# Optimization experiments

Measured on AMD Instinct MI355X. Metric: run time of the kernel, lower is better.

Reference implementation:

```python
import jax, jax.numpy as jnp
import numpy as np

N_NODES, N_EDGES = 50000, 800000
IN_DIM, OUT_DIM, EDGE_DIM = 128, 128, 32
NUM_HEADS = 8
HEAD_DIM = OUT_DIM // NUM_HEADS
SCALE = HEAD_DIM ** -0.5


def setup_inputs() -> dict:
    key = jax.random.key(0)
    ks = jax.random.split(key, 8)
    def lin_w(k, fan_in, fan_out):
        # kaiming-uniform-ish init like nn.Linear
        bound = 1.0 / np.sqrt(fan_in)
        return jax.random.uniform(k, (fan_in, fan_out), jnp.float32, -bound, bound)
    return {
        "node_features": jax.random.normal(ks[0], (N_NODES, IN_DIM), jnp.float32),
        "edge_features": jax.random.normal(ks[1], (N_EDGES, EDGE_DIM), jnp.float32),
        "Wq": lin_w(ks[2], IN_DIM, OUT_DIM), "bq": jnp.zeros((OUT_DIM,), jnp.float32),
        "Wk": lin_w(ks[3], IN_DIM, OUT_DIM), "bk": jnp.zeros((OUT_DIM,), jnp.float32),
        "Wv": lin_w(ks[4], IN_DIM, OUT_DIM), "bv": jnp.zeros((OUT_DIM,), jnp.float32),
        "We": lin_w(ks[5], EDGE_DIM, OUT_DIM), "be": jnp.zeros((OUT_DIM,), jnp.float32),
        "edge_list": jax.random.randint(ks[6], (N_EDGES, 2), 0, N_NODES, jnp.int32),
        "num_nodes": N_NODES,
    }


def reference(node_features, edge_features, Wq, bq, Wk, bk, Wv, bv, We, be, edge_list, num_nodes):
    # node projections -> [N, H, D]
    Q = (node_features @ Wq + bq).reshape(-1, NUM_HEADS, HEAD_DIM)
    K = (node_features @ Wk + bk).reshape(-1, NUM_HEADS, HEAD_DIM)
    V = (node_features @ Wv + bv).reshape(-1, NUM_HEADS, HEAD_DIM)
    edge_bias = (edge_features @ We + be).reshape(-1, NUM_HEADS, HEAD_DIM)

    src = edge_list[:, 0]  # node_in
    dst = edge_list[:, 1]  # node_out

    # per-edge per-head scores: [E, H]
    scores = jnp.einsum("ehd,ehd->eh", Q[src], K[dst]) * SCALE + edge_bias.sum(-1)
    # NOTE: softmax over the HEADS axis (dim=1), exactly as in the source
    weights = jax.nn.softmax(scores, axis=1)

    # weighted messages gathered from src, scattered to dst: [E, H, D] -> [N, H, D]
    msg = V[src] * weights[..., None]
    node_updates = jax.ops.segment_sum(msg, dst, num_segments=num_nodes)
    return node_updates.reshape(num_nodes, OUT_DIM)
```

## Files before the change

### kernel.cpp

```cpp
#include <hip/hip_runtime.h>
#include <math.h>

#define IN_DIM   128
#define OUT_DIM  128
#define EDGE_DIM 32
#define NUM_HEADS 8
#define HEAD_DIM 16
#define SCALE 0.25f
#define CSTRIDE 16
#define MAXDEG 48

typedef __attribute__((ext_vector_type(8))) short bf16x8;
typedef __attribute__((ext_vector_type(4))) float f32x4;
typedef __attribute__((ext_vector_type(2))) float f32x2;
typedef __attribute__((ext_vector_type(4))) unsigned int u32x4;

__device__ inline unsigned short f2bf(float x) {
    unsigned int u = __float_as_uint(x);
    unsigned int r = u + 0x7fff + ((u >> 16) & 1);
    return (unsigned short)(r >> 16);
}
__device__ inline float bflo(unsigned int u) { return __uint_as_float(u << 16); }
__device__ inline float bfhi(unsigned int u) { return __uint_as_float(u & 0xffff0000u); }
__device__ inline f32x2 up2(unsigned int u) {
    f32x2 r; r[0] = bflo(u); r[1] = bfhi(u); return r;
}

__global__ __launch_bounds__(256) void setup_kernel(
    int* __restrict__ counts, int n_nodes, int nbz,
    const float* __restrict__ Wq, const float* __restrict__ Wk,
    const float* __restrict__ Wv, unsigned short* __restrict__ WtB, int nbw,
    const float* __restrict__ We, const float* __restrict__ be,
    float* __restrict__ WeR, float* __restrict__ beR)
{
    const int bx = blockIdx.x;
    const int t  = threadIdx.x;
    if (bx < nbz) {
        const int i = bx * 256 + t;
        if (i < n_nodes) counts[i << 4] = 0;
    } else if (bx < nbz + nbw) {
        const int idx = (bx - nbz) * 256 + t;
        const int mat = idx >> 14;
        const int rem = idx & 16383;
        const int n = rem >> 7, k = rem & 127;
        const float* W = (mat == 0) ? Wq : (mat == 1) ? Wk : Wv;
        WtB[mat * 16384 + n * 128 + k] = f2bf(W[k * 128 + n]);
    } else {
        const int k = t >> 3, h = t & 7;
        float s = 0.f;
#pragma unroll
        for (int d = 0; d < HEAD_DIM; ++d) s += We[k * OUT_DIM + h * HEAD_DIM + d];
        WeR[k * NUM_HEADS + h] = s;
        if (t < NUM_HEADS) {
            float sb = 0.f;
#pragma unroll
            for (int d = 0; d < HEAD_DIM; ++d) sb += be[t * HEAD_DIM + d];
            beR[t] = sb;
        }
    }
}

__global__ __launch_bounds__(256) void mega_kernel(
    const float* __restrict__ X, const unsigned short* __restrict__ WtB,
    const float* __restrict__ bq, const float* __restrict__ bk,
    const float* __restrict__ bv,
    unsigned short* __restrict__ QVb, unsigned short* __restrict__ Kb,
    int n_nodes, int nbm,
    const int* __restrict__ el, int* __restrict__ counts,
    const float* __restrict__ ef, const float* __restrict__ WeR,
    const float* __restrict__ beR, unsigned int* __restrict__ recs,
    int n_edges)
{
    __shared__ unsigned short shW[16384];
    const int bx = blockIdx.x;
    const int t  = threadIdx.x;
    const int ngemm = 3 * nbm;

    if (bx >= ngemm) {
        const int e = (bx - ngemm) * 256 + t;
        if (e >= n_edges) return;
        const int2 ed = ((const int2*)el)[e];
        const int r = atomicAdd(&counts[ed.y << 4], 1);

        float acc[NUM_HEADS];
#pragma unroll
        for (int h = 0; h < NUM_HEADS; ++h) acc[h] = beR[h];

        const f32x4* efr = (const f32x4*)(ef + (size_t)e * EDGE_DIM);
#pragma unroll
        for (int kk = 0; kk < 8; ++kk) {
            const f32x4 f = efr[kk];
#pragma unroll
            for (int c = 0; c < 4; ++c) {
                const float* wr = WeR + (kk * 4 + c) * NUM_HEADS;
#pragma unroll
                for (int h = 0; h < NUM_HEADS; ++h)
                    acc[h] = fmaf(f[c], wr[h], acc[h]);
            }
        }

        if (r < MAXDEG) {
            u32x4 r0, r1;
            r0[0] = (unsigned)ed.x;
            r0[1] = 0;
            r0[2] = (unsigned)f2bf(acc[0]) | ((unsigned)f2bf(acc[1]) << 16);
            r0[3] = (unsigned)f2bf(acc[2]) | ((unsigned)f2bf(acc[3]) << 16);
            r1[0] = (unsigned)f2bf(acc[4]) | ((unsigned)f2bf(acc[5]) << 16);
            r1[1] = (unsigned)f2bf(acc[6]) | ((unsigned)f2bf(acc[7]) << 16);
            r1[2] = 0; r1[3] = 0;
            u32x4* rp = (u32x4*)(recs + (size_t)(ed.y * MAXDEG + r) * 8);
            rp[0] = r0;
            rp[1] = r1;
        }
        return;
    }

    const int which = bx / nbm;
    const int mb    = bx - which * nbm;
    const unsigned short* Wg = WtB + which * 16384;

#pragma unroll
    for (int kk = 0; kk < 8; ++kk) {
        const int c = kk * 256 + t;
        const u32x4 v = ((const u32x4*)Wg)[c];
        const int row = c >> 4;
        const int bir = (c & 15) << 4;
        *(u32x4*)((char*)shW + row * 256 + (bir ^ ((row & 7) << 4))) = v;
    }
    __syncthreads();

    const int wave = t >> 6, lane = t & 63;
    const int quad = lane >> 4, li = lane & 15;
    const int mbase = mb * 256 + wave * 64;

    int mrow[4];
#pragma unroll
    for (int m = 0; m < 4; ++m) {
        const int r_ = mbase + m * 16 + li;
        mrow[m] = (r_ < n_nodes) ? r_ : (n_nodes - 1);
    }

    f32x4 acc[4][8];
#pragma unroll
    for (int m = 0; m < 4; ++m)
#pragma unroll
        for (int nt = 0; nt < 8; ++nt) acc[m][nt] = (f32x4){0.f, 0.f, 0.f, 0.f};

#pragma unroll
    for (int ks = 0; ks < 4; ++ks) {
        bf16x8 a[4];
#pragma unroll
        for (int m = 0; m < 4; ++m) {
            const f32x4* xr = (const f32x4*)(X + (size_t)mrow[m] * 128 + ks * 32 + quad * 8);
            const f32x4 x0 = xr[0], x1 = xr[1];
            bf16x8 av;
            av[0] = (short)f2bf(x0[0]); av[1] = (short)f2bf(x0[1]);
            av[2] = (short)f2bf(x0[2]); av[3] = (short)f2bf(x0[3]);
            av[4] = (short)f2bf(x1[0]); av[5] = (short)f2bf(x1[1]);
            av[6] = (short)f2bf(x1[2]); av[7] = (short)f2bf(x1[3]);
            a[m] = av;
        }
#pragma unroll
        for (int nt = 0; nt < 8; ++nt) {
            const int row = nt * 16 + li;
            const bf16x8 b = *(const bf16x8*)((const char*)shW + row * 256 +
                                ((ks * 64 + quad * 16) ^ ((row & 7) << 4)));
#pragma unroll
            for (int m = 0; m < 4; ++m)
                acc[m][nt] = __builtin_amdgcn_mfma_f32_16x16x32_bf16(a[m], b, acc[m][nt], 0, 0, 0);
        }
    }

    const float* bias = (which == 0) ? bq : (which == 1) ? bk : bv;
    float bv8[8];
#pragma unroll
    for (int nt = 0; nt < 8; ++nt) bv8[nt] = bias[nt * 16 + li];

    __syncthreads();

    unsigned short* stg = shW + wave * 2176;
    const int R = lane >> 2, cc4 = lane & 3;
#pragma unroll
    for (int m = 0; m < 4; ++m) {
#pragma unroll
        for (int nt = 0; nt < 8; ++nt)
#pragma unroll
            for (int r = 0; r < 4; ++r)
                stg[(quad * 4 + r) * 136 + nt * 16 + li] = f2bf(acc[m][nt][r] + bv8[nt]);
        __syncthreads();

        const int node = mbase + m * 16 + R;
        if (node < n_nodes) {
            const u32x4* s = (const u32x4*)(stg + R * 136 + cc4 * 32);
            u32x4 d0 = s[0], d1 = s[1], d2 = s[2], d3 = s[3];
            unsigned short* dp =
                (which == 0) ? (QVb + (size_t)node * 256 + cc4 * 32)
              : (which == 1) ? (Kb  + (size_t)node * 128 + cc4 * 32)
              :                (QVb + (size_t)node * 256 + 128 + cc4 * 32);
            u32x4* d = (u32x4*)dp;
            d[0] = d0; d[1] = d1; d[2] = d2; d[3] = d3;
        }
        __syncthreads();
    }
}

__global__ __launch_bounds__(256) void aggregate_kernel(
    const unsigned short* __restrict__ QVb, const unsigned short* __restrict__ Kb,
    const int* __restrict__ counts, const unsigned int* __restrict__ recs,
    float* __restrict__ out, int n_nodes, int nwtot)
{
    const int lane = threadIdx.x & 63;
    const int g = lane >> 3;
    const int h = lane & 7;
    const int ebd = 2 + (h >> 1);

    int node = (blockIdx.x * 256 + threadIdx.x) >> 6;
    if (node >= n_nodes) return;
    int cnt = counts[node << 4];
    if (cnt > MAXDEG) cnt = MAXDEG;

    for (;;) {
        const int nnode = node + nwtot;
        int ncnt = 0;
        if (nnode < n_nodes) {
            ncnt = counts[nnode << 4];
            if (ncnt > MAXDEG) ncnt = MAXDEG;
        }

        const int beg = node * MAXDEG;

        f32x2 kf[8];
        {
            const u32x4* kp = (const u32x4*)(Kb + (size_t)node * 128 + h * 16);
            const u32x4 ka = kp[0], kb_ = kp[1];
#pragma unroll
            for (int j = 0; j < 4; ++j) { kf[j] = up2(ka[j]); kf[4 + j] = up2(kb_[j]); }
        }

        f32x2 acc[8];
#pragma unroll
        for (int j = 0; j < 8; ++j) acc[j] = (f32x2){0.f, 0.f};

        if (cnt > 0) {
            const int last = cnt - 1;
            int s0 = g; if (s0 > last) s0 = last;
            const unsigned src_c = recs[(size_t)(beg + s0) * 8];
            unsigned ebw_c = recs[(size_t)(beg + s0) * 8 + ebd];
            const unsigned short* bp0 = QVb + (size_t)src_c * 256 + h * 16;
            u32x4 qa = *(const u32x4*)bp0;
            u32x4 qb = *(const u32x4*)(bp0 + 8);
            u32x4 va = *(const u32x4*)(bp0 + 128);
            u32x4 vb = *(const u32x4*)(bp0 + 136);
            int s1 = 8 + g; if (s1 > last) s1 = last;
            unsigned src_n = recs[(size_t)(beg + s1) * 8];
            unsigned ebw_n = recs[(size_t)(beg + s1) * 8 + ebd];

            for (int i = 0; i < cnt; i += 8) {
                int s2 = i + 16 + g; if (s2 > last) s2 = last;
                const unsigned src_f = recs[(size_t)(beg + s2) * 8];
                const unsigned ebw_f = recs[(size_t)(beg + s2) * 8 + ebd];
                const unsigned short* bp = QVb + (size_t)src_n * 256 + h * 16;
                const u32x4 qan = *(const u32x4*)bp;
                const u32x4 qbn = *(const u32x4*)(bp + 8);
                const u32x4 van = *(const u32x4*)(bp + 128);
                const u32x4 vbn = *(const u32x4*)(bp + 136);

                const float eb = (h & 1) ? bfhi(ebw_c) : bflo(ebw_c);
                f32x2 p2 = (f32x2){0.f, 0.f};
#pragma unroll
                for (int j = 0; j < 4; ++j) {
                    p2 += up2(qa[j]) * kf[j];
                    p2 += up2(qb[j]) * kf[4 + j];
                }
                const float score = fmaf(p2[0] + p2[1], SCALE, eb);

                const float ex = __expf(score);
                float den = ex;
                den += __shfl_xor(den, 1);
                den += __shfl_xor(den, 2);
                den += __shfl_xor(den, 4);
                float wgt = __fdividef(ex, den);
                if (i + g >= cnt) wgt = 0.f;
                const f32x2 w2 = (f32x2){wgt, wgt};
#pragma unroll
                for (int j = 0; j < 4; ++j) {
                    acc[j]     += up2(va[j]) * w2;
                    acc[4 + j] += up2(vb[j]) * w2;
                }

                qa = qan; qb = qbn; va = van; vb = vbn;
                ebw_c = ebw_n;
                src_n = src_f; ebw_n = ebw_f;
            }
        }

#pragma unroll
        for (int mask = 8; mask <= 32; mask <<= 1)
#pragma unroll
            for (int j = 0; j < 8; ++j) {
                f32x2 o;
                o[0] = __shfl_xor(acc[j][0], mask);
                o[1] = __shfl_xor(acc[j][1], mask);
                acc[j] += o;
            }

        float ox = 0.f, oy = 0.f;
#pragma unroll
        for (int j = 0; j < 8; ++j)
            if (g == j) { ox = acc[j][0]; oy = acc[j][1]; }
        *(float2*)(out + (size_t)node * OUT_DIM + h * 16 + g * 2) = make_float2(ox, oy);

        if (nnode >= n_nodes) break;
        node = nnode; cnt = ncnt;
    }
}

extern "C" void kernel_launch(void* const* d_in, const int* in_sizes, int n_in,
                              void* d_out, int out_size, void* d_ws, size_t ws_size,
                              hipStream_t stream)
{
    const float* X   = (const float*)d_in[0];
    const float* ef  = (const float*)d_in[1];
    const float* Wq  = (const float*)d_in[2];
    const float* bq  = (const float*)d_in[3];
    const float* Wk  = (const float*)d_in[4];
    const float* bk  = (const float*)d_in[5];
    const float* Wv  = (const float*)d_in[6];
    const float* bv  = (const float*)d_in[7];
    const float* We  = (const float*)d_in[8];
    const float* be  = (const float*)d_in[9];
    const int*   el  = (const int*)d_in[10];

    const int n_nodes = in_sizes[0] / IN_DIM;
    const int n_edges = in_sizes[10] / 2;

    char* w = (char*)d_ws;
    auto alloc = [&](size_t bytes) { char* p = w; w += (bytes + 255) & ~(size_t)255; return p; };

    unsigned short* QVb  = (unsigned short*)alloc((size_t)n_nodes * 256 * 2);
    unsigned short* Kb   = (unsigned short*)alloc((size_t)n_nodes * 128 * 2);
    unsigned short* WtB  = (unsigned short*)alloc((size_t)3 * 128 * 128 * 2);
    unsigned int*   recs = (unsigned int*)alloc((size_t)n_nodes * MAXDEG * 32);
    float* WeR   = (float*)alloc(EDGE_DIM * NUM_HEADS * 4);
    float* beR   = (float*)alloc(NUM_HEADS * 4);
    int* counts  = (int*)alloc((size_t)n_nodes * CSTRIDE * 4);

    const int nbz = (n_nodes + 255) / 256;
    const int nbw = (3 * 128 * 128) / 256;
    setup_kernel<<<nbz + nbw + 1, 256, 0, stream>>>(
        counts, n_nodes, nbz, Wq, Wk, Wv, WtB, nbw, We, be, WeR, beR);

    const int nbm = (n_nodes + 255) / 256;
    const int nbh = (n_edges + 255) / 256;
    mega_kernel<<<3 * nbm + nbh, 256, 0, stream>>>(
        X, WtB, bq, bk, bv, QVb, Kb, n_nodes, nbm,
        el, counts, ef, WeR, beR, recs, n_edges);

    int nblk = (n_nodes + 3) / 4;
    if (nblk > 2048) nblk = 2048;
    aggregate_kernel<<<nblk, 256, 0, stream>>>(
        QVb, Kb, counts, recs, (float*)d_out, n_nodes, nblk * 4);
}
```

Measured before the change: 313.7 us.

## Pre-convert node features to bf16 and split fused GEMM/edge kernel

Adds a bf16 conversion pass for the node features in the setup kernel, writing into the records buffer as scratch, so the QKV GEMM reads bf16 directly instead of re-reading and converting fp32 for each of the three projections. The former fused kernel is split into a separate QKV GEMM kernel and an edge-record kernel. This cuts the feature read traffic in the GEMM from three fp32 passes to one fp32 pass plus three bf16 passes. In exchange it adds one kernel launch and loses the overlap between GEMM blocks and edge blocks. It relies on the QKV kernel finishing before the edge kernel overwrites the reused buffer.

Measured after the change: 331.4 us. +5.6%, slower.

```diff
diff --git a/kernel.cpp b/kernel.cpp
--- a/kernel.cpp
+++ b/kernel.cpp
@@ -31,7 +31,8 @@
     const float* __restrict__ Wq, const float* __restrict__ Wk,
     const float* __restrict__ Wv, unsigned short* __restrict__ WtB, int nbw,
     const float* __restrict__ We, const float* __restrict__ be,
-    float* __restrict__ WeR, float* __restrict__ beR)
+    float* __restrict__ WeR, float* __restrict__ beR,
+    const float* __restrict__ X, unsigned short* __restrict__ Xb)
 {
     const int bx = blockIdx.x;
     const int t  = threadIdx.x;
@@ -45,7 +46,7 @@
         const int n = rem >> 7, k = rem & 127;
         const float* W = (mat == 0) ? Wq : (mat == 1) ? Wk : Wv;
         WtB[mat * 16384 + n * 128 + k] = f2bf(W[k * 128 + n]);
-    } else {
+    } else if (bx == nbz + nbw) {
         const int k = t >> 3, h = t & 7;
         float s = 0.f;
 #pragma unroll
@@ -57,63 +58,31 @@
             for (int d = 0; d < HEAD_DIM; ++d) sb += be[t * HEAD_DIM + d];
             beR[t] = sb;
         }
-    }
-}
-
-__global__ __launch_bounds__(256) void mega_kernel(
-    const float* __restrict__ X, const unsigned short* __restrict__ WtB,
+    } else {
+        const int i = (bx - (nbz + nbw + 1)) * 256 + t;
+        if (i < n_nodes * 16) {
+            const f32x4* xr = (const f32x4*)(X + (size_t)i * 8);
+            const f32x4 x0 = xr[0], x1 = xr[1];
+            u32x4 p;
+            p[0] = (unsigned)f2bf(x0[0]) | ((unsigned)f2bf(x0[1]) << 16);
+            p[1] = (unsigned)f2bf(x0[2]) | ((unsigned)f2bf(x0[3]) << 16);
+            p[2] = (unsigned)f2bf(x1[0]) | ((unsigned)f2bf(x1[1]) << 16);
+            p[3] = (unsigned)f2bf(x1[2]) | ((unsigned)f2bf(x1[3]) << 16);
+            *(u32x4*)(Xb + (size_t)i * 8) = p;
+        }
+    }
+}
+
+__global__ __launch_bounds__(256) void qkv_kernel(
+    const unsigned short* __restrict__ Xb, const unsigned short* __restrict__ WtB,
     const float* __restrict__ bq, const float* __restrict__ bk,
     const float* __restrict__ bv,
     unsigned short* __restrict__ QVb, unsigned short* __restrict__ Kb,
-    int n_nodes, int nbm,
-    const int* __restrict__ el, int* __restrict__ counts,
-    const float* __restrict__ ef, const float* __restrict__ WeR,
-    const float* __restrict__ beR, unsigned int* __restrict__ recs,
-    int n_edges)
+    int n_nodes, int nbm)
 {
     __shared__ unsigned short shW[16384];
     const int bx = blockIdx.x;
     const int t  = threadIdx.x;
-    const int ngemm = 3 * nbm;
-
-    if (bx >= ngemm) {
-        const int e = (bx - ngemm) * 256 + t;
-        if (e >= n_edges) return;
-        const int2 ed = ((const int2*)el)[e];
-        const int r = atomicAdd(&counts[ed.y << 4], 1);
-
-        float acc[NUM_HEADS];
-#pragma unroll
-        for (int h = 0; h < NUM_HEADS; ++h) acc[h] = beR[h];
-
-        const f32x4* efr = (const f32x4*)(ef + (size_t)e * EDGE_DIM);
-#pragma unroll
-        for (int kk = 0; kk < 8; ++kk) {
-            const f32x4 f = efr[kk];
-#pragma unroll
-            for (int c = 0; c < 4; ++c) {
-                const float* wr = WeR + (kk * 4 + c) * NUM_HEADS;
-#pragma unroll
-                for (int h = 0; h < NUM_HEADS; ++h)
-                    acc[h] = fmaf(f[c], wr[h], acc[h]);
-            }
-        }
-
-        if (r < MAXDEG) {
-            u32x4 r0, r1;
-            r0[0] = (unsigned)ed.x;
-            r0[1] = 0;
-            r0[2] = (unsigned)f2bf(acc[0]) | ((unsigned)f2bf(acc[1]) << 16);
-            r0[3] = (unsigned)f2bf(acc[2]) | ((unsigned)f2bf(acc[3]) << 16);
-            r1[0] = (unsigned)f2bf(acc[4]) | ((unsigned)f2bf(acc[5]) << 16);
-            r1[1] = (unsigned)f2bf(acc[6]) | ((unsigned)f2bf(acc[7]) << 16);
-            r1[2] = 0; r1[3] = 0;
-            u32x4* rp = (u32x4*)(recs + (size_t)(ed.y * MAXDEG + r) * 8);
-            rp[0] = r0;
-            rp[1] = r1;
-        }
-        return;
-    }
 
     const int which = bx / nbm;
     const int mb    = bx - which * nbm;
@@ -150,16 +119,8 @@
     for (int ks = 0; ks < 4; ++ks) {
         bf16x8 a[4];
 #pragma unroll
-        for (int m = 0; m < 4; ++m) {
-            const f32x4* xr = (const f32x4*)(X + (size_t)mrow[m] * 128 + ks * 32 + quad * 8);
-            const f32x4 x0 = xr[0], x1 = xr[1];
-            bf16x8 av;
-            av[0] = (short)f2bf(x0[0]); av[1] = (short)f2bf(x0[1]);
-            av[2] = (short)f2bf(x0[2]); av[3] = (short)f2bf(x0[3]);
-            av[4] = (short)f2bf(x1[0]); av[5] = (short)f2bf(x1[1]);
-            av[6] = (short)f2bf(x1[2]); av[7] = (short)f2bf(x1[3]);
-            a[m] = av;
-        }
+        for (int m = 0; m < 4; ++m)
+            a[m] = *(const bf16x8*)(Xb + (size_t)mrow[m] * 128 + ks * 32 + quad * 8);
 #pragma unroll
         for (int nt = 0; nt < 8; ++nt) {
             const int row = nt * 16 + li;
@@ -201,6 +162,49 @@
             d[0] = d0; d[1] = d1; d[2] = d2; d[3] = d3;
         }
         __syncthreads();
+    }
+}
+
+__global__ __launch_bounds__(256) void edge_kernel(
+    const int* __restrict__ el, int* __restrict__ counts,
+    const float* __restrict__ ef, const float* __restrict__ WeR,
+    const float* __restrict__ beR, unsigned int* __restrict__ recs,
+    int n_edges)
+{
+    const int e = blockIdx.x * 256 + threadIdx.x;
+    if (e >= n_edges) return;
+    const int2 ed = ((const int2*)el)[e];
+    const int r = atomicAdd(&counts[ed.y << 4], 1);
+
+    float acc[NUM_HEADS];
+#pragma unroll
+    for (int h = 0; h < NUM_HEADS; ++h) acc[h] = beR[h];
+
+    const f32x4* efr = (const f32x4*)(ef + (size_t)e * EDGE_DIM);
+#pragma unroll
+    for (int kk = 0; kk < 8; ++kk) {
+        const f32x4 f = efr[kk];
+#pragma unroll
+        for (int c = 0; c < 4; ++c) {
+            const float* wr = WeR + (kk * 4 + c) * NUM_HEADS;
+#pragma unroll
+            for (int h = 0; h < NUM_HEADS; ++h)
+                acc[h] = fmaf(f[c], wr[h], acc[h]);
+        }
+    }
+
+    if (r < MAXDEG) {
+        u32x4 r0, r1;
+        r0[0] = (unsigned)ed.x;
+        r0[1] = 0;
+        r0[2] = (unsigned)f2bf(acc[0]) | ((unsigned)f2bf(acc[1]) << 16);
+        r0[3] = (unsigned)f2bf(acc[2]) | ((unsigned)f2bf(acc[3]) << 16);
+        r1[0] = (unsigned)f2bf(acc[4]) | ((unsigned)f2bf(acc[5]) << 16);
+        r1[1] = (unsigned)f2bf(acc[6]) | ((unsigned)f2bf(acc[7]) << 16);
+        r1[2] = 0; r1[3] = 0;
+        u32x4* rp = (u32x4*)(recs + (size_t)(ed.y * MAXDEG + r) * 8);
+        rp[0] = r0;
+        rp[1] = r1;
     }
 }
 
@@ -345,15 +349,20 @@
     float* beR   = (float*)alloc(NUM_HEADS * 4);
     int* counts  = (int*)alloc((size_t)n_nodes * CSTRIDE * 4);
 
+    unsigned short* Xb = (unsigned short*)recs;
+
     const int nbz = (n_nodes + 255) / 256;
     const int nbw = (3 * 128 * 128) / 256;
-    setup_kernel<<<nbz + nbw + 1, 256, 0, stream>>>(
-        counts, n_nodes, nbz, Wq, Wk, Wv, WtB, nbw, We, be, WeR, beR);
+    const int nbx = (n_nodes * 16 + 255) / 256;
+    setup_kernel<<<nbz + nbw + 1 + nbx, 256, 0, stream>>>(
+        counts, n_nodes, nbz, Wq, Wk, Wv, WtB, nbw, We, be, WeR, beR, X, Xb);
 
     const int nbm = (n_nodes + 255) / 256;
+    qkv_kernel<<<3 * nbm, 256, 0, stream>>>(
+        Xb, WtB, bq, bk, bv, QVb, Kb, n_nodes, nbm);
+
     const int nbh = (n_edges + 255) / 256;
-    mega_kernel<<<3 * nbm + nbh, 256, 0, stream>>>(
-        X, WtB, bq, bk, bv, QVb, Kb, n_nodes, nbm,
+    edge_kernel<<<nbh, 256, 0, stream>>>(
         el, counts, ef, WeR, beR, recs, n_edges);
 
     int nblk = (n_nodes + 3) / 4;
```
